# Kernel tuning notes

Hardware: AMD Instinct MI355X
Metric: run time of the kernel (lower is better)

The kernel has to match this reference:

```python
import jax, jax.numpy as jnp
import numpy as np

B, T, D = 4, 2048, 1024
H = 16
DH = D // H


def setup_inputs() -> dict:
    key = jax.random.key(0)
    ks = jax.random.split(key, 5)
    s = 1.0 / np.sqrt(D)
    x = jax.random.normal(ks[0], (B, T, D), dtype=jnp.float32)
    w_qkv = jax.random.uniform(ks[1], (3 * D, D), dtype=jnp.float32, minval=-s, maxval=s)
    b_qkv = jax.random.uniform(ks[2], (3 * D,), dtype=jnp.float32, minval=-s, maxval=s)
    w_out = jax.random.uniform(ks[3], (D, D), dtype=jnp.float32, minval=-s, maxval=s)
    b_out = jax.random.uniform(ks[4], (D,), dtype=jnp.float32, minval=-s, maxval=s)
    return {"x": x, "w_qkv": w_qkv, "b_qkv": b_qkv, "w_out": w_out, "b_out": b_out}


def reference(x, w_qkv, b_qkv, w_out, b_out):
    Bq, Tq, C = x.shape
    scale = jnp.asarray(np.sqrt(DH), dtype=x.dtype)
    qkv = x @ w_qkv.T + b_qkv                      # [B,T,3D]
    qkv = qkv.reshape(Bq, Tq, 3, H, DH)
    qkv = jnp.transpose(qkv, (2, 0, 3, 1, 4))      # [3,B,H,T,DH]
    q, k, v = qkv[0], qkv[1], qkv[2]
    attn = jnp.einsum('bhqd,bhkd->bhqk', q, k) / scale
    attn = jax.nn.softmax(attn, axis=-1)
    out = jnp.einsum('bhqk,bhkd->bhqd', attn, v)   # [B,H,T,DH]
    out = jnp.transpose(out, (0, 2, 1, 3)).reshape(Bq, Tq, C)
    return out @ w_out.T + b_out
```

## Files before the change

kernel.cpp:

```cpp
#include <hip/hip_runtime.h>
#include <stdint.h>

typedef __attribute__((ext_vector_type(8))) short bf16x8;
typedef __attribute__((ext_vector_type(4))) short s16x4;
typedef __attribute__((ext_vector_type(4))) float f32x4;

#define DEV static __device__ __forceinline__

DEV short f2bf(float f) {
    union { float f; uint32_t u; } v; v.f = f;
    uint32_t r = (v.u + 0x7fffu + ((v.u >> 16) & 1u)) >> 16;
    return (short)r;
}

DEV void gll16(const void* g, void* l) {
    __builtin_amdgcn_global_load_lds(
        (const __attribute__((address_space(1))) uint32_t*)g,
        (__attribute__((address_space(3))) uint32_t*)l, 16, 0, 0);
}

DEV void wait_vm0()   { asm volatile("s_waitcnt vmcnt(0)" ::: "memory"); }
DEV void wait_vm4()   { asm volatile("s_waitcnt vmcnt(4)" ::: "memory"); }
DEV void wait_lgkm0() { asm volatile("s_waitcnt lgkmcnt(0)" ::: "memory"); }

__global__ __launch_bounds__(256) void k_convert(
    const float* __restrict__ x,  short* __restrict__ xb,
    const float* __restrict__ wq, short* __restrict__ wqb,
    const float* __restrict__ wo, short* __restrict__ wob)
{
    const int NX = (8192*1024)/4, NW = (3072*1024)/4, NO = (1024*1024)/4;
    const int total = NX + NW + NO;
    for (int i = blockIdx.x*blockDim.x + threadIdx.x; i < total; i += gridDim.x*blockDim.x) {
        const float* s; short* d; int j;
        if (i < NX)           { s = x;  d = xb;  j = i; }
        else if (i < NX + NW) { s = wq; d = wqb; j = i - NX; }
        else                  { s = wo; d = wob; j = i - NX - NW; }
        f32x4 v = *(const f32x4*)(s + (size_t)j*4);
        s16x4 o;
        o[0] = f2bf(v[0]); o[1] = f2bf(v[1]); o[2] = f2bf(v[2]); o[3] = f2bf(v[3]);
        *(s16x4*)(d + (size_t)j*4) = o;
    }
}

template<int MODE>
__global__ __launch_bounds__(256) void k_gemm(
    const short* __restrict__ A,
    const short* __restrict__ Bw,
    const float* __restrict__ bias,
    void* __restrict__ Cout,
    void* __restrict__ Cout2,
    int Nld, int K)
{
    __shared__ short smem[17408];
    short* As = smem;
    short* Bs = smem + 8192;
    const int tid = threadIdx.x;
    const int l = tid & 63, w = tid >> 6;
    const int bm = blockIdx.x << 7, bn = blockIdx.y << 7;
    const int wm = (w >> 1) << 6, wn = (w & 1) << 6;
    const int l15 = l & 15, lh = l >> 4;
    const int rS = tid >> 3, cS = tid & 7;

    f32x4 acc[4][4] = {};
    const int KT = K >> 6;

    for (int kt = 0; kt < KT; ++kt) {
        const int k0 = kt << 6;
        #pragma unroll
        for (int rr = 0; rr < 4; ++rr) {
            int r = (rr << 5) + rS;
            int cs = (cS ^ (r & 7)) << 3;
            gll16(A  + (size_t)(bm + r)*K + k0 + cs, As + ((rr<<8) + tid)*8);
            gll16(Bw + (size_t)(bn + r)*K + k0 + cs, Bs + ((rr<<8) + tid)*8);
        }
        wait_vm0();
        __syncthreads();

        bf16x8 af[2][4], bfr[2][4];
        #pragma unroll
        for (int ks = 0; ks < 2; ++ks) {
            #pragma unroll
            for (int mf = 0; mf < 4; ++mf) {
                int r = wm + (mf << 4) + l15;
                int cc = ((ks << 5) + (lh << 3)) ^ ((r & 7) << 3);
                af[ks][mf] = *(const bf16x8*)(As + r*64 + cc);
            }
            #pragma unroll
            for (int nf = 0; nf < 4; ++nf) {
                int r = wn + (nf << 4) + l15;
                int cc = ((ks << 5) + (lh << 3)) ^ ((r & 7) << 3);
                bfr[ks][nf] = *(const bf16x8*)(Bs + r*64 + cc);
            }
        }
        #pragma unroll
        for (int ks = 0; ks < 2; ++ks)
            #pragma unroll
            for (int mf = 0; mf < 4; ++mf)
                #pragma unroll
                for (int nf = 0; nf < 4; ++nf)
                    acc[mf][nf] = __builtin_amdgcn_mfma_f32_16x16x32_bf16(
                        af[ks][mf], bfr[ks][nf], acc[mf][nf], 0, 0, 0);
        __syncthreads();
    }

    float bv[4];
    #pragma unroll
    for (int nf = 0; nf < 4; ++nf) bv[nf] = bias[bn + wn + (nf<<4) + l15];

    if (MODE == 0) {
        #pragma unroll
        for (int mf = 0; mf < 4; ++mf)
            #pragma unroll
            for (int nf = 0; nf < 4; ++nf)
                #pragma unroll
                for (int v = 0; v < 4; ++v) {
                    int r = wm + (mf<<4) + (lh<<2) + v;
                    int c = wn + (nf<<4) + l15;
                    smem[r*136 + c] = f2bf(acc[mf][nf][v] + bv[nf]);
                }
        __syncthreads();
        if (bn < 2048) {
            int r = tid >> 1, half = tid & 1;
            const short* src = smem + r*136 + (half << 6);
            short* dst = (short*)Cout + (size_t)(bm + r)*2048 + bn + (half << 6);
            #pragma unroll
            for (int c = 0; c < 8; ++c)
                *(bf16x8*)(dst + (c<<3)) = *(const bf16x8*)(src + (c<<3));
        } else {
            int nl = tid >> 1;
            int nloc = (bn - 2048) + nl;
            int hh = nloc >> 6, d = nloc & 63;
            int tl0 = (tid & 1) << 6;
            int bb = bm >> 11;
            int tt0 = (bm & 2047) + tl0;
            short* dst = (short*)Cout2 + (((size_t)((bb << 4) + hh) << 6) + d) * 2048 + tt0;
            #pragma unroll
            for (int c = 0; c < 8; ++c) {
                bf16x8 pk;
                #pragma unroll
                for (int j = 0; j < 8; ++j)
                    pk[j] = smem[(tl0 + (c<<3) + j)*136 + nl];
                *(bf16x8*)(dst + (c<<3)) = pk;
            }
        }
    } else {
        float* C = (float*)Cout;
        #pragma unroll
        for (int mf = 0; mf < 4; ++mf)
            #pragma unroll
            for (int nf = 0; nf < 4; ++nf)
                #pragma unroll
                for (int v = 0; v < 4; ++v) {
                    int r = bm + wm + (mf<<4) + (lh<<2) + v;
                    int c = bn + wn + (nf<<4) + l15;
                    C[(size_t)r*Nld + c] = acc[mf][nf][v] + bv[nf];
                }
    }
}

__global__ __launch_bounds__(256) void k_attn(
    const short* __restrict__ qk, const short* __restrict__ Vt,
    short* __restrict__ Ob)
{
    __shared__ short Kd[2][4096];
    __shared__ short Vs[2][4096];
    __shared__ short Pl[4][2048];

    const int tid = threadIdx.x;
    const int l = tid & 63, w = tid >> 6;
    const int l15 = l & 15, lh = l >> 4;
    const int qt0 = blockIdx.x << 7;
    const int bh = blockIdx.y;
    const int b = bh >> 4, h = bh & 15;
    const short* Qbase = qk + (size_t)(b << 11) * 2048 + (h << 6);
    const short* Kbase = Qbase + 1024;
    const short* Vtg = Vt + ((size_t)bh << 17);
    short* Plw = &Pl[w][0];
    const int rS = tid >> 3, cS = tid & 7;

    bf16x8 qfr[2][2];
    #pragma unroll
    for (int qf = 0; qf < 2; ++qf)
        #pragma unroll
        for (int ks = 0; ks < 2; ++ks) {
            int t = qt0 + (w << 5) + (qf << 4) + l15;
            qfr[qf][ks] = *(const bf16x8*)(Qbase + (size_t)t*2048 + (ks << 5) + (lh << 3));
        }

    f32x4 o[2][4] = {};
    float mr[2], sr[2];
    mr[0] = mr[1] = -__builtin_inff();
    sr[0] = sr[1] = 0.f;
    const float SCALE = 0.125f * 1.44269504088896341f;

    auto stage = [&](int kv0, int buf) {
        #pragma unroll
        for (int rr = 0; rr < 2; ++rr) {
            int r = (rr << 5) + rS;
            int cs = (cS ^ (r & 7)) << 3;
            gll16(Kbase + (size_t)(kv0 + r)*2048 + cs, &Kd[buf][((rr<<8) + tid)*8]);
            gll16(Vtg + ((size_t)r << 11) + kv0 + cs,  &Vs[buf][((rr<<8) + tid)*8]);
        }
    };

    auto tile_compute = [&](int cur) {
        f32x4 p2[4][2] = {};
        #pragma unroll
        for (int ks = 0; ks < 2; ++ks)
            #pragma unroll
            for (int mf = 0; mf < 4; ++mf) {
                int r = (mf << 4) + l15;
                int cc = ((ks << 5) + (lh << 3)) ^ ((r & 7) << 3);
                bf16x8 kf = *(const bf16x8*)(&Kd[cur][r*64 + cc]);
                #pragma unroll
                for (int qf = 0; qf < 2; ++qf)
                    p2[mf][qf] = __builtin_amdgcn_mfma_f32_16x16x32_bf16(
                        kf, qfr[qf][ks], p2[mf][qf], 0, 0, 0);
            }

        #pragma unroll
        for (int qf = 0; qf < 2; ++qf) {
            float mt = p2[0][qf][0];
            #pragma unroll
            for (int mf = 0; mf < 4; ++mf)
                #pragma unroll
                for (int v = 0; v < 4; ++v)
                    if (mf | v) mt = fmaxf(mt, p2[mf][qf][v]);
            mt = fmaxf(mt, __shfl_xor(mt, 16));
            mt = fmaxf(mt, __shfl_xor(mt, 32));
            float mnew = fmaxf(mr[qf], mt * SCALE);
            float alpha = exp2f(mr[qf] - mnew);
            mr[qf] = mnew;
            float ts = 0.f;
            #pragma unroll
            for (int mf = 0; mf < 4; ++mf)
                #pragma unroll
                for (int v = 0; v < 4; ++v) {
                    float e = exp2f(p2[mf][qf][v] * SCALE - mnew);
                    p2[mf][qf][v] = e;
                    ts += e;
                }
            ts += __shfl_xor(ts, 16);
            ts += __shfl_xor(ts, 32);
            sr[qf] = sr[qf] * alpha + ts;
            #pragma unroll
            for (int df = 0; df < 4; ++df)
                #pragma unroll
                for (int v = 0; v < 4; ++v)
                    o[qf][df][v] *= alpha;
            int row = (qf << 4) + l15;
            int rs = (row & 7) << 3;
            #pragma unroll
            for (int mf = 0; mf < 4; ++mf) {
                s16x4 st;
                #pragma unroll
                for (int v = 0; v < 4; ++v)
                    st[v] = f2bf(p2[mf][qf][v]);
                *(s16x4*)(Plw + row*64 + (((mf << 4) + (lh << 2)) ^ rs)) = st;
            }
        }

        wait_lgkm0();
        bf16x8 pa[2][2];
        #pragma unroll
        for (int ks = 0; ks < 2; ++ks)
            #pragma unroll
            for (int qf = 0; qf < 2; ++qf) {
                int r = (qf << 4) + l15;
                int cc = ((ks << 5) + (lh << 3)) ^ ((r & 7) << 3);
                pa[ks][qf] = *(const bf16x8*)(Plw + r*64 + cc);
            }
        #pragma unroll
        for (int ks = 0; ks < 2; ++ks)
            #pragma unroll
            for (int df = 0; df < 4; ++df) {
                int r = (df << 4) + l15;
                int cc = ((ks << 5) + (lh << 3)) ^ ((r & 7) << 3);
                bf16x8 vb = *(const bf16x8*)(&Vs[cur][r*64 + cc]);
                #pragma unroll
                for (int qf = 0; qf < 2; ++qf)
                    o[qf][df] = __builtin_amdgcn_mfma_f32_16x16x32_bf16(
                        vb, pa[ks][qf], o[qf][df], 0, 0, 0);
            }
    };

    stage(0, 0);
    for (int it = 0; it < 31; ++it) {
        int cur = it & 1;
        stage((it + 1) << 6, cur ^ 1);
        wait_vm4();
        __syncthreads();
        tile_compute(cur);
        __syncthreads();
    }
    wait_vm0();
    __syncthreads();
    tile_compute(1);

    #pragma unroll
    for (int qf = 0; qf < 2; ++qf) {
        float inv = 1.0f / sr[qf];
        int t = qt0 + (w << 5) + (qf << 4) + l15;
        short* rowp = Ob + (size_t)((b << 11) + t) * 1024 + (h << 6);
        #pragma unroll
        for (int df = 0; df < 4; ++df) {
            s16x4 st;
            #pragma unroll
            for (int v = 0; v < 4; ++v)
                st[v] = f2bf(o[qf][df][v] * inv);
            *(s16x4*)(rowp + (df << 4) + (lh << 2)) = st;
        }
    }
}

extern "C" void kernel_launch(void* const* d_in, const int* in_sizes, int n_in,
                              void* d_out, int out_size, void* d_ws, size_t ws_size,
                              hipStream_t stream)
{
    const float* x     = (const float*)d_in[0];
    const float* w_qkv = (const float*)d_in[1];
    const float* b_qkv = (const float*)d_in[2];
    const float* w_out = (const float*)d_in[3];
    const float* b_out = (const float*)d_in[4];
    float* out = (float*)d_out;

    short* qk  = (short*)d_ws;
    short* Vt  = qk  + (size_t)8192*2048;
    short* wqb = Vt  + (size_t)64*64*2048;
    short* wob = wqb + (size_t)3072*1024;
    short* xb  = wob + (size_t)1024*1024;
    short* Ob  = xb;

    k_convert<<<2048, 256, 0, stream>>>(x, xb, w_qkv, wqb, w_out, wob);
    k_gemm<0><<<dim3(64, 24), 256, 0, stream>>>(xb, wqb, b_qkv, (void*)qk, (void*)Vt, 2048, 1024);
    k_attn<<<dim3(16, 64), 256, 0, stream>>>(qk, Vt, Ob);
    k_gemm<1><<<dim3(64, 8), 256, 0, stream>>>(Ob, wob, b_out, (void*)out, (void*)nullptr, 1024, 1024);
}
```

Baseline: 364.0 us.

## Add lazy softmax rescaling, hardware bf16 pack, fast exp2 and GEMM block swizzle

The attention softmax now rescales the running max, sum and output accumulator only when a wave sees a new max more than 8 above the stored one. It uses the raw hardware exp2 builtin and converts probabilities with the v_cvt_pk_bf16_f32 instruction instead of a manual rounding routine. Max and sum reductions become balanced trees to shorten dependency chains. The GEMM kernels remap block indices so neighbouring blocks share tiles, for better L2 locality. The lazy rescale lets exponentials reach up to 2^8 before renormalisation, which relies on fp32 and bf16 headroom, and the swizzle hardcodes a 64-wide grid in x.

```diff
diff --git a/kernel.cpp b/kernel.cpp
--- a/kernel.cpp
+++ b/kernel.cpp
@@ -4,6 +4,7 @@
 typedef __attribute__((ext_vector_type(8))) short bf16x8;
 typedef __attribute__((ext_vector_type(4))) short s16x4;
 typedef __attribute__((ext_vector_type(4))) float f32x4;
+typedef __attribute__((ext_vector_type(2))) int i32x2;
 
 #define DEV static __device__ __forceinline__
 
@@ -12,6 +13,14 @@
     uint32_t r = (v.u + 0x7fffu + ((v.u >> 16) & 1u)) >> 16;
     return (short)r;
 }
+
+DEV int cvtpk(float lo, float hi) {
+    int r;
+    asm("v_cvt_pk_bf16_f32 %0, %1, %2" : "=v"(r) : "v"(lo), "v"(hi));
+    return r;
+}
+
+DEV float exp2n(float x) { return __builtin_amdgcn_exp2f(x); }
 
 DEV void gll16(const void* g, void* l) {
     __builtin_amdgcn_global_load_lds(
@@ -56,7 +65,10 @@
     short* Bs = smem + 8192;
     const int tid = threadIdx.x;
     const int l = tid & 63, w = tid >> 6;
-    const int bm = blockIdx.x << 7, bn = blockIdx.y << 7;
+    const int lin = blockIdx.y * 64 + blockIdx.x;
+    const int per = (gridDim.y << 6) >> 3;
+    const int idx = (lin & 7) * per + (lin >> 3);
+    const int bm = (idx & 63) << 7, bn = (idx >> 6) << 7;
     const int wm = (w >> 1) << 6, wn = (w & 1) << 6;
     const int l15 = l & 15, lh = l >> 4;
     const int rS = tid >> 3, cS = tid & 7;
@@ -220,43 +232,51 @@
 
         #pragma unroll
         for (int qf = 0; qf < 2; ++qf) {
-            float mt = p2[0][qf][0];
-            #pragma unroll
-            for (int mf = 0; mf < 4; ++mf)
-                #pragma unroll
-                for (int v = 0; v < 4; ++v)
-                    if (mf | v) mt = fmaxf(mt, p2[mf][qf][v]);
+            float ma = fmaxf(fmaxf(p2[0][qf][0], p2[0][qf][1]),
+                             fmaxf(p2[0][qf][2], p2[0][qf][3]));
+            float mb = fmaxf(fmaxf(p2[1][qf][0], p2[1][qf][1]),
+                             fmaxf(p2[1][qf][2], p2[1][qf][3]));
+            float mc = fmaxf(fmaxf(p2[2][qf][0], p2[2][qf][1]),
+                             fmaxf(p2[2][qf][2], p2[2][qf][3]));
+            float md = fmaxf(fmaxf(p2[3][qf][0], p2[3][qf][1]),
+                             fmaxf(p2[3][qf][2], p2[3][qf][3]));
+            float mt = fmaxf(fmaxf(ma, mb), fmaxf(mc, md));
             mt = fmaxf(mt, __shfl_xor(mt, 16));
             mt = fmaxf(mt, __shfl_xor(mt, 32));
-            float mnew = fmaxf(mr[qf], mt * SCALE);
-            float alpha = exp2f(mr[qf] - mnew);
-            mr[qf] = mnew;
-            float ts = 0.f;
-            #pragma unroll
-            for (int mf = 0; mf < 4; ++mf)
-                #pragma unroll
-                for (int v = 0; v < 4; ++v) {
-                    float e = exp2f(p2[mf][qf][v] * SCALE - mnew);
-                    p2[mf][qf][v] = e;
-                    ts += e;
-                }
+            float mts = mt * SCALE;
+            if (__any(mts > mr[qf] + 8.0f)) {
+                float mnew = fmaxf(mr[qf], mts);
+                float alpha = exp2n(mr[qf] - mnew);
+                mr[qf] = mnew;
+                sr[qf] *= alpha;
+                #pragma unroll
+                for (int df = 0; df < 4; ++df)
+                    #pragma unroll
+                    for (int v = 0; v < 4; ++v)
+                        o[qf][df][v] *= alpha;
+            }
+            float m_use = mr[qf];
+            float tsp[4];
+            #pragma unroll
+            for (int mf = 0; mf < 4; ++mf) {
+                #pragma unroll
+                for (int v = 0; v < 4; ++v)
+                    p2[mf][qf][v] = exp2n(p2[mf][qf][v] * SCALE - m_use);
+                tsp[mf] = (p2[mf][qf][0] + p2[mf][qf][1]) +
+                          (p2[mf][qf][2] + p2[mf][qf][3]);
+            }
+            float ts = (tsp[0] + tsp[1]) + (tsp[2] + tsp[3]);
             ts += __shfl_xor(ts, 16);
             ts += __shfl_xor(ts, 32);
-            sr[qf] = sr[qf] * alpha + ts;
-            #pragma unroll
-            for (int df = 0; df < 4; ++df)
-                #pragma unroll
-                for (int v = 0; v < 4; ++v)
-                    o[qf][df][v] *= alpha;
+            sr[qf] += ts;
             int row = (qf << 4) + l15;
             int rs = (row & 7) << 3;
             #pragma unroll
             for (int mf = 0; mf < 4; ++mf) {
-                s16x4 st;
-                #pragma unroll
-                for (int v = 0; v < 4; ++v)
-                    st[v] = f2bf(p2[mf][qf][v]);
-                *(s16x4*)(Plw + row*64 + (((mf << 4) + (lh << 2)) ^ rs)) = st;
+                i32x2 dw;
+                dw[0] = cvtpk(p2[mf][qf][0], p2[mf][qf][1]);
+                dw[1] = cvtpk(p2[mf][qf][2], p2[mf][qf][3]);
+                *(i32x2*)(Plw + row*64 + (((mf << 4) + (lh << 2)) ^ rs)) = dw;
             }
         }
 
```

After: 331.7 us. 8.9% less time.
